# Kernel optimization log

Measured on AMD Instinct MI355X. Metric: run time of the kernel, lower is better.

## Reference

```python
import jax, jax.numpy as jnp
import numpy as np

V, N, K, D = 2, 100000, 8, 128
TAU = 1.0
LOG_2PI = float(np.log(2.0 * np.pi))


def setup_inputs() -> dict:
    key = jax.random.key(0)
    k1, k2, k3 = jax.random.split(key, 3)
    z = jax.random.normal(k1, (V, N, D), dtype=jnp.float32)
    phi = jnp.ones((V, K), dtype=jnp.float32) / K
    mu = jax.random.normal(k2, (V, K, D), dtype=jnp.float32)
    # sigma: identity (as in torch init) plus a small symmetric PSD perturbation
    a = 0.05 * jax.random.normal(k3, (V, K, D, D), dtype=jnp.float32)
    sigma = jnp.eye(D, dtype=jnp.float32) + jnp.einsum('vkde,vkfe->vkdf', a, a)
    return {"z": z, "phi": phi, "mu": mu, "sigma": sigma}


def _compute_energy(z, phi, mu, sigma):
    # z: [N, D]; phi: [K]; mu: [K, D]; sigma: [K, D, D]
    eps_eye = 1e-6 * jnp.eye(D, dtype=z.dtype)
    sigma_stable = sigma + eps_eye  # [K, D, D]
    inv_sigma = jnp.linalg.inv(sigma_stable)
    det_sigma = jnp.clip(jnp.linalg.det(sigma_stable), 1e-6, None)  # [K]
    diff = z[:, None, :] - mu[None, :, :]  # [N, K, D]
    maha = jnp.einsum('nkd,kde,nke->nk', diff, inv_sigma, diff)  # [N, K]
    log_pi = jax.nn.log_softmax(phi)  # [K]
    log_prob = (-0.5 * maha
                - 0.5 * D * LOG_2PI
                - 0.5 * jnp.log(det_sigma)[None, :]
                + log_pi[None, :])  # [N, K]
    energy = -jax.nn.logsumexp(log_prob, axis=1)  # [N]
    penalty = jnp.sum(1.0 / (jnp.diagonal(sigma_stable, axis1=-2, axis2=-1) + 1e-12))
    return energy, penalty


def reference(z, phi, mu, sigma):
    # vmap over views; energies_v: [V, N]
    energies_v, penalties = jax.vmap(_compute_energy)(z, phi, mu, sigma)
    energies = energies_v.T  # [N, V]
    total_energies = jnp.sum(energies)
    total_penalty = jnp.sum(penalties)
    weights = jax.nn.softmax(-energies / TAU, axis=1)  # [N, V]
    return energies, weights, total_energies, total_penalty
```

## Files before the change

### kernel.cpp

```cpp
#include <hip/hip_runtime.h>
#include <math.h>

#define V 2
#define NN 100000
#define KK 8
#define DD 128
#define TILE_N 128
#define SL 132
#define NT 782
#define CH 8
#define NCHUNK 98
#define NPAD 100096
#define LOG2PI 1.8378770664093454f
#define LOG_1EM6 -13.815510557964274f

#define IMG_B 69632
#define IMG_HALF 17408
#define LF_B   1114112
#define BV_B   2228224
#define C_B    2236416
#define MAHA_B 2236480

#define OUT_W_OFF (NN*V)
#define OUT_TE (2*NN*V)
#define OUT_TP (2*NN*V + 1)

typedef __attribute__((ext_vector_type(8))) short bf16x8;
typedef __attribute__((ext_vector_type(4))) float f32x4;

__device__ __forceinline__ unsigned short f2bf_rtn(float f) {
    unsigned u = __builtin_bit_cast(unsigned, f);
    unsigned r = u + 0x7FFFu + ((u >> 16) & 1u);
    return (unsigned short)(r >> 16);
}
__device__ __forceinline__ float bf2f(unsigned short h) {
    unsigned u = ((unsigned)h) << 16;
    return __builtin_bit_cast(float, u);
}

__global__ void zero_kernel(float* out) {
    int t = threadIdx.x;
    if (t < 2) out[OUT_TE + t] = 0.0f;
}

__global__ __launch_bounds__(256) void prep_chol(const float* __restrict__ phi,
                                                 const float* __restrict__ mu,
                                                 const float* __restrict__ sigma,
                                                 void* __restrict__ wsv,
                                                 float* __restrict__ out) {
    __shared__ float Lf[DD * SL];
    __shared__ float P[8][SL];
    __shared__ float dvec[DD];
    __shared__ float mulds[DD];
    __shared__ float red[256];
    __shared__ float Bv[8];
    __shared__ float Bb[DD];

    const int tid = threadIdx.x;
    const int vk  = blockIdx.x;
    const int v   = vk >> 3;
    const int k   = vk & 7;
    const int R   = tid >> 4;
    const int C   = tid & 15;

    if (tid < DD) mulds[tid] = mu[vk * DD + tid];

    float A[8][8];
    const float* sig = sigma + (size_t)vk * DD * DD;
    float pen = 0.0f;
    #pragma unroll
    for (int a = 0; a < 8; ++a) {
        const float4* p4 = (const float4*)(sig + (size_t)(8 * R + a) * DD + 8 * C);
        float4 x = p4[0], y = p4[1];
        A[a][0] = x.x; A[a][1] = x.y; A[a][2] = x.z; A[a][3] = x.w;
        A[a][4] = y.x; A[a][5] = y.y; A[a][6] = y.z; A[a][7] = y.w;
        if (R == C) A[a][a] += 1e-6f;
    }
    if (R == C) {
        #pragma unroll
        for (int a = 0; a < 8; ++a) pen += 1.0f / (A[a][a] + 1e-12f);
    }

    for (int i = tid; i < DD * SL; i += 256) Lf[i] = 0.0f;

    red[tid] = pen;
    __syncthreads();
    for (int s = 128; s > 0; s >>= 1) {
        if (tid < s) red[tid] += red[tid + s];
        __syncthreads();
    }
    if (tid == 0) atomicAdd(&out[OUT_TP], red[0]);
    __syncthreads();

    for (int p = 0; p < 16; ++p) {
        if (C == p && R >= p) {
            #pragma unroll
            for (int b = 0; b < 8; ++b) {
                *(float4*)&P[b][8 * R]     = make_float4(A[0][b], A[1][b], A[2][b], A[3][b]);
                *(float4*)&P[b][8 * R + 4] = make_float4(A[4][b], A[5][b], A[6][b], A[7][b]);
            }
        }
        __syncthreads();

        if (tid < 64) {
            const int lane = tid;
            const int r1 = 8 * p + lane;
            const int r2 = r1 + 64;
            const bool ok2 = (r2 < DD);
            float pr1[8], pr2[8], rs[8];
            #pragma unroll
            for (int j = 0; j < 8; ++j) {
                pr1[j] = (r1 < DD) ? P[j][r1] : 0.0f;
                pr2[j] = ok2 ? P[j][r2] : 0.0f;
            }
            #pragma unroll
            for (int j = 0; j < 8; ++j) {
                if (lane >= j && lane < 8) Bv[lane] = pr1[j];
                __builtin_amdgcn_wave_barrier();
                float bv[8];
                #pragma unroll
                for (int m = 0; m < 8; ++m) bv[m] = Bv[m];
                __builtin_amdgcn_wave_barrier();
                float piv = bv[j];
                if (lane == j) dvec[8 * p + j] = piv;
                float inv2 = 1.0f / piv;
                rs[j] = rsqrtf(piv);
                float m1 = pr1[j] * inv2;
                float m2 = pr2[j] * inv2;
                #pragma unroll
                for (int j2 = 0; j2 < 8; ++j2) {
                    if (j2 > j) {
                        if (lane > j) pr1[j2] -= m1 * bv[j2];
                        pr2[j2] -= m2 * bv[j2];
                    }
                }
            }
            #pragma unroll
            for (int j = 0; j < 8; ++j) {
                if (r1 < DD) {
                    float v1 = (lane >= j) ? pr1[j] * rs[j] : 0.0f;
                    P[j][r1] = v1;
                    Lf[r1 * SL + 8 * p + j] = v1;
                }
                if (ok2) {
                    float v2 = pr2[j] * rs[j];
                    P[j][r2] = v2;
                    Lf[r2 * SL + 8 * p + j] = v2;
                }
            }
        }
        __syncthreads();

        if (C > p && R >= p) {
            #pragma unroll
            for (int j = 0; j < 8; ++j) {
                float4 a0 = *(const float4*)&P[j][8 * R];
                float4 a1 = *(const float4*)&P[j][8 * R + 4];
                float4 b0 = *(const float4*)&P[j][8 * C];
                float4 b1 = *(const float4*)&P[j][8 * C + 4];
                float ra[8] = {a0.x, a0.y, a0.z, a0.w, a1.x, a1.y, a1.z, a1.w};
                float rb[8] = {b0.x, b0.y, b0.z, b0.w, b1.x, b1.y, b1.z, b1.w};
                #pragma unroll
                for (int a = 0; a < 8; ++a)
                    #pragma unroll
                    for (int b = 0; b < 8; ++b)
                        A[a][b] -= ra[a] * rb[b];
            }
        }
        __syncthreads();
    }

    if (tid < 64) {
        const int lane = tid;
        float acc0 = mulds[lane];
        float acc1 = mulds[lane + 64];
        for (int j = 0; j < DD; ++j) {
            if (j < 64) { if (lane == j)      Bb[j] = acc0 / Lf[j * SL + j]; }
            else        { if (lane == j - 64) Bb[j] = acc1 / Lf[j * SL + j]; }
            __builtin_amdgcn_wave_barrier();
            float bj = Bb[j];
            __builtin_amdgcn_wave_barrier();
            if (lane > j)      acc0 -= Lf[lane * SL + j] * bj;
            if (lane + 64 > j) acc1 -= Lf[(lane + 64) * SL + j] * bj;
        }
    }
    __syncthreads();
    if (tid < DD) ((float*)((char*)wsv + BV_B))[vk * DD + tid] = Bb[tid];

    {
        float4* Lg = (float4*)((char*)wsv + LF_B + (size_t)vk * IMG_B);
        const float4* Ls4 = (const float4*)Lf;
        for (int i = tid; i < DD * SL / 4; i += 256) Lg[i] = Ls4[i];
    }

    red[tid] = (tid < DD) ? logf(dvec[tid]) : 0.0f;
    __syncthreads();
    for (int s = 128; s > 0; s >>= 1) {
        if (tid < s) red[tid] += red[tid + s];
        __syncthreads();
    }
    if (tid == 0) {
        float logdet_c = fmaxf(red[0], LOG_1EM6);
        const float* ph = phi + v * KK;
        float m = ph[0];
        for (int i = 1; i < KK; ++i) m = fmaxf(m, ph[i]);
        float s = 0.0f;
        for (int i = 0; i < KK; ++i) s += expf(ph[i] - m);
        float logpi = ph[k] - m - logf(s);
        ((float*)((char*)wsv + C_B))[vk] = logpi - 0.5f * logdet_c - 0.5f * (float)DD * LOG2PI;
    }
}

__global__ __launch_bounds__(256) void prep_trsm(void* __restrict__ wsv) {
    __shared__ float Ls[DD * SL];
    __shared__ float Wc[32][SL];

    const int tid = threadIdx.x;
    const int vk  = blockIdx.x >> 2;
    const int cg  = blockIdx.x & 3;

    const float4* Lg = (const float4*)((const char*)wsv + LF_B + (size_t)vk * IMG_B);
    float4* Ls4 = (float4*)Ls;
    for (int i = tid; i < DD * SL / 4; i += 256) Ls4[i] = Lg[i];
    __syncthreads();

    const int c   = tid >> 3;
    const int par = tid & 7;
    const int j   = 4 * c + cg;

    for (int e = par; e < SL; e += 8) Wc[c][e] = 0.0f;
    if (par == 0) Wc[c][j] = 1.0f / Ls[j * SL + j];
    __builtin_amdgcn_wave_barrier();

    const int pbase = j & ~3;
    for (int i = j + 1; i < DD; ++i) {
        float s = 0.0f;
        for (int p4 = pbase + 4 * par; p4 < i; p4 += 32) {
            float4 lf = *(const float4*)&Ls[i * SL + p4];
            float4 wc = *(const float4*)&Wc[c][p4];
            s += lf.x * wc.x + lf.y * wc.y + lf.z * wc.z + lf.w * wc.w;
        }
        s += __shfl_xor(s, 1, 64);
        s += __shfl_xor(s, 2, 64);
        s += __shfl_xor(s, 4, 64);
        if (par == 0) Wc[c][i] = -s / Ls[i * SL + i];
        __builtin_amdgcn_wave_barrier();
    }

    unsigned short* Gh = (unsigned short*)((char*)wsv + (size_t)vk * IMG_B);
    unsigned short* Gl = Gh + IMG_HALF;
    for (int i2 = par; i2 < DD; i2 += 8) {
        float f = (i2 >= j) ? Wc[c][i2] : 0.0f;
        unsigned short h = f2bf_rtn(f);
        unsigned short l = f2bf_rtn(f - bf2f(h));
        Gh[i2 * 136 + j] = h;
        Gl[i2 * 136 + j] = l;
    }
}

__global__ __launch_bounds__(256, 2) void maha_kernel(const float* __restrict__ z,
                                                      void* __restrict__ wsv) {
    __shared__ unsigned short wl[IMG_B / 2];
    __shared__ float bl_s[DD];

    const int tid  = threadIdx.x;
    const int lane = tid & 63;
    const int wave = tid >> 6;
    const int quad = lane >> 4;
    const int l16  = lane & 15;
    const int r     = blockIdx.y;
    const int chunk = blockIdx.x;
    const int vv    = r >> 3;

    {
        const char* src = (const char*)wsv + (size_t)r * IMG_B;
        char* dst = (char*)wl;
        const int lane_off = wave * 1024 + lane * 16;
        #pragma unroll
        for (int t = 0; t < 17; ++t)
            __builtin_amdgcn_global_load_lds(
                (const __attribute__((address_space(1))) void*)(src + t * 4096 + lane_off),
                (__attribute__((address_space(3))) void*)(dst + t * 4096 + wave * 1024),
                16, 0, 0);
    }
    if (tid < DD) bl_s[tid] = ((const float*)((const char*)wsv + BV_B))[r * DD + tid];
    __syncthreads();

    const float* zbase = z + (size_t)vv * NN * DD;
    float* mrow = (float*)((char*)wsv + MAHA_B) + (size_t)r * NPAD;

    for (int ti = 0; ti < CH; ++ti) {
        const int t = chunk * CH + ti;
        if (t >= NT) break;
        const int n0 = t * TILE_N;

        bf16x8 zhi[2][4], zlo[2][4];
        #pragma unroll
        for (int mt = 0; mt < 2; ++mt) {
            int n = n0 + wave * 32 + mt * 16 + l16;
            bool ok = (n < NN);
            const float* zp = zbase + (size_t)n * DD + quad * 8;
            #pragma unroll
            for (int ds = 0; ds < 4; ++ds) {
                float f[8];
                if (ok) {
                    float4 a  = *(const float4*)(zp + ds * 32);
                    float4 bq = *(const float4*)(zp + ds * 32 + 4);
                    f[0] = a.x;  f[1] = a.y;  f[2] = a.z;  f[3] = a.w;
                    f[4] = bq.x; f[5] = bq.y; f[6] = bq.z; f[7] = bq.w;
                } else {
                    #pragma unroll
                    for (int e = 0; e < 8; ++e) f[e] = 0.0f;
                }
                bf16x8 hi8, lo8;
                #pragma unroll
                for (int e = 0; e < 8; ++e) {
                    unsigned short hu = f2bf_rtn(f[e]);
                    unsigned short lu = f2bf_rtn(f[e] - bf2f(hu));
                    hi8[e] = (short)hu;
                    lo8[e] = (short)lu;
                }
                zhi[mt][ds] = hi8;
                zlo[mt][ds] = lo8;
            }
        }

        f32x4 acc[2][8];
        #pragma unroll
        for (int mt = 0; mt < 2; ++mt)
            #pragma unroll
            for (int nt = 0; nt < 8; ++nt)
                acc[mt][nt] = (f32x4)(0.0f);

        #pragma unroll
        for (int ds = 0; ds < 4; ++ds) {
            const int g = ds * 4 + quad;
            #pragma unroll
            for (int nt = 0; nt < 8; ++nt) {
                if (nt < 2 * ds) continue;
                int row = nt * 16 + l16;
                int off = row * 136 + g * 8;
                bf16x8 bh  = *(const bf16x8*)&wl[off];
                bf16x8 blo = *(const bf16x8*)&wl[IMG_HALF + off];
                #pragma unroll
                for (int mt = 0; mt < 2; ++mt) {
                    acc[mt][nt] = __builtin_amdgcn_mfma_f32_16x16x32_bf16(zhi[mt][ds], bh,  acc[mt][nt], 0, 0, 0);
                    acc[mt][nt] = __builtin_amdgcn_mfma_f32_16x16x32_bf16(zhi[mt][ds], blo, acc[mt][nt], 0, 0, 0);
                    acc[mt][nt] = __builtin_amdgcn_mfma_f32_16x16x32_bf16(zlo[mt][ds], bh,  acc[mt][nt], 0, 0, 0);
                }
            }
        }

        #pragma unroll
        for (int mt = 0; mt < 2; ++mt) {
            float p[4] = {0.f, 0.f, 0.f, 0.f};
            #pragma unroll
            for (int nt = 0; nt < 8; ++nt) {
                float bc = bl_s[nt * 16 + l16];
                f32x4 a = acc[mt][nt];
                float y0 = a[0] - bc, y1 = a[1] - bc, y2 = a[2] - bc, y3 = a[3] - bc;
                p[0] += y0 * y0; p[1] += y1 * y1; p[2] += y2 * y2; p[3] += y3 * y3;
            }
            float sv[4];
            #pragma unroll
            for (int reg = 0; reg < 4; ++reg) {
                float s = p[reg];
                s += __shfl_xor(s, 1, 64);
                s += __shfl_xor(s, 2, 64);
                s += __shfl_xor(s, 4, 64);
                s += __shfl_xor(s, 8, 64);
                sv[reg] = s;
            }
            if (l16 == 0)
                *(float4*)&mrow[n0 + wave * 32 + mt * 16 + quad * 4] =
                    make_float4(sv[0], sv[1], sv[2], sv[3]);
        }
    }
}

__global__ __launch_bounds__(256) void finalize_kernel(const void* __restrict__ wsv,
                                                       float* __restrict__ out) {
    __shared__ float red[256];
    __shared__ float clds[16];

    const int tid = threadIdx.x;
    if (tid < 16) clds[tid] = ((const float*)((const char*)wsv + C_B))[tid];
    __syncthreads();

    const float* mahap = (const float*)((const char*)wsv + MAHA_B);
    const int n = blockIdx.x * 256 + tid;
    float esum = 0.0f;

    if (n < NN) {
        float ev[V];
        #pragma unroll
        for (int vv = 0; vv < V; ++vv) {
            float lp[KK];
            float m = -1e30f;
            #pragma unroll
            for (int k = 0; k < KK; ++k) {
                int r = vv * KK + k;
                lp[k] = -0.5f * mahap[(size_t)r * NPAD + n] + clds[r];
                m = fmaxf(m, lp[k]);
            }
            float s = 0.0f;
            #pragma unroll
            for (int k = 0; k < KK; ++k) s += expf(lp[k] - m);
            ev[vv] = -(m + logf(s));
        }
        float e0 = ev[0], e1 = ev[1];
        float m = fmaxf(-e0, -e1);
        float x0 = expf(-e0 - m);
        float x1 = expf(-e1 - m);
        float inv = 1.0f / (x0 + x1);
        out[(size_t)n * V + 0] = e0;
        out[(size_t)n * V + 1] = e1;
        out[OUT_W_OFF + (size_t)n * V + 0] = x0 * inv;
        out[OUT_W_OFF + (size_t)n * V + 1] = x1 * inv;
        esum = e0 + e1;
    }

    red[tid] = esum;
    __syncthreads();
    for (int s = 128; s > 0; s >>= 1) {
        if (tid < s) red[tid] += red[tid + s];
        __syncthreads();
    }
    if (tid == 0) atomicAdd(&out[OUT_TE], red[0]);
}

extern "C" void kernel_launch(void* const* d_in, const int* in_sizes, int n_in,
                              void* d_out, int out_size, void* d_ws, size_t ws_size,
                              hipStream_t stream) {
    const float* z     = (const float*)d_in[0];
    const float* phi   = (const float*)d_in[1];
    const float* mu    = (const float*)d_in[2];
    const float* sigma = (const float*)d_in[3];
    float* out = (float*)d_out;

    hipLaunchKernelGGL(zero_kernel, dim3(1), dim3(64), 0, stream, out);
    hipLaunchKernelGGL(prep_chol, dim3(V * KK), dim3(256), 0, stream, phi, mu, sigma, d_ws, out);
    hipLaunchKernelGGL(prep_trsm, dim3(64), dim3(256), 0, stream, d_ws);
    hipLaunchKernelGGL(maha_kernel, dim3(NCHUNK, 16), dim3(256), 0, stream, z, d_ws);
    hipLaunchKernelGGL(finalize_kernel, dim3((NPAD + 255) / 256), dim3(256), 0, stream, d_ws, out);
}
```

Measured before the change: 400.3 us.

## Double maha tile to 512 threads, interleave z conversion per k-slice, cheaper bf16 split

The maha kernel now launches 512-thread blocks over 256-row tiles, so each staged LDS image of the triangular factor is reused by twice as many rows, and launch bounds allow four blocks per CU. The z load and bf16 hi/lo split move inside the k-slice loop, which cuts live registers. The split now uses a truncate-plus-round perm sequence instead of two round-to-nearest conversions. This lowers register pressure and conversion ALU work, but the hi part is now truncated, not rounded, which slightly changes numerics. The LDS image copy loop is also rewritten for 8 waves.

```diff
diff --git a/kernel.cpp b/kernel.cpp
--- a/kernel.cpp
+++ b/kernel.cpp
@@ -5,12 +5,12 @@
 #define NN 100000
 #define KK 8
 #define DD 128
-#define TILE_N 128
+#define TILE_N 256
 #define SL 132
-#define NT 782
-#define CH 8
+#define NT 391
+#define CH 4
 #define NCHUNK 98
-#define NPAD 100096
+#define NPAD 100352
 #define LOG2PI 1.8378770664093454f
 #define LOG_1EM6 -13.815510557964274f
 
@@ -27,6 +27,7 @@
 
 typedef __attribute__((ext_vector_type(8))) short bf16x8;
 typedef __attribute__((ext_vector_type(4))) float f32x4;
+typedef __attribute__((ext_vector_type(4))) unsigned u32x4;
 
 __device__ __forceinline__ unsigned short f2bf_rtn(float f) {
     unsigned u = __builtin_bit_cast(unsigned, f);
@@ -36,6 +37,17 @@
 __device__ __forceinline__ float bf2f(unsigned short h) {
     unsigned u = ((unsigned)h) << 16;
     return __builtin_bit_cast(float, u);
+}
+
+__device__ __forceinline__ void cvt_pair(float f0, float f1, unsigned& hi, unsigned& lo) {
+    unsigned u0 = __builtin_bit_cast(unsigned, f0);
+    unsigned u1 = __builtin_bit_cast(unsigned, f1);
+    hi = __builtin_amdgcn_perm(u1, u0, 0x07060302u);
+    float r0 = f0 - __builtin_bit_cast(float, u0 & 0xFFFF0000u);
+    float r1 = f1 - __builtin_bit_cast(float, u1 & 0xFFFF0000u);
+    unsigned v0 = __builtin_bit_cast(unsigned, r0) + 0x8000u;
+    unsigned v1 = __builtin_bit_cast(unsigned, r1) + 0x8000u;
+    lo = __builtin_amdgcn_perm(v1, v0, 0x07060302u);
 }
 
 __global__ void zero_kernel(float* out) {
@@ -258,7 +270,7 @@
     }
 }
 
-__global__ __launch_bounds__(256, 2) void maha_kernel(const float* __restrict__ z,
+__global__ __launch_bounds__(512, 4) void maha_kernel(const float* __restrict__ z,
                                                       void* __restrict__ wsv) {
     __shared__ unsigned short wl[IMG_B / 2];
     __shared__ float bl_s[DD];
@@ -275,13 +287,17 @@
     {
         const char* src = (const char*)wsv + (size_t)r * IMG_B;
         char* dst = (char*)wl;
-        const int lane_off = wave * 1024 + lane * 16;
-        #pragma unroll
-        for (int t = 0; t < 17; ++t)
-            __builtin_amdgcn_global_load_lds(
-                (const __attribute__((address_space(1))) void*)(src + t * 4096 + lane_off),
-                (__attribute__((address_space(3))) void*)(dst + t * 4096 + wave * 1024),
-                16, 0, 0);
+        const int woff = wave * 1024;
+        const int lane_off = woff + lane * 16;
+        #pragma unroll
+        for (int t = 0; t < 9; ++t) {
+            if (t * 8192 + woff < IMG_B) {
+                __builtin_amdgcn_global_load_lds(
+                    (const __attribute__((address_space(1))) void*)(src + t * 8192 + lane_off),
+                    (__attribute__((address_space(3))) void*)(dst + t * 8192 + woff),
+                    16, 0, 0);
+            }
+        }
     }
     if (tid < DD) bl_s[tid] = ((const float*)((const char*)wsv + BV_B))[r * DD + tid];
     __syncthreads();
@@ -290,63 +306,56 @@
     float* mrow = (float*)((char*)wsv + MAHA_B) + (size_t)r * NPAD;
 
     for (int ti = 0; ti < CH; ++ti) {
-        const int t = chunk * CH + ti;
-        if (t >= NT) break;
+        const int t  = chunk * CH + ti;
         const int n0 = t * TILE_N;
 
-        bf16x8 zhi[2][4], zlo[2][4];
-        #pragma unroll
-        for (int mt = 0; mt < 2; ++mt) {
-            int n = n0 + wave * 32 + mt * 16 + l16;
-            bool ok = (n < NN);
-            const float* zp = zbase + (size_t)n * DD + quad * 8;
-            #pragma unroll
-            for (int ds = 0; ds < 4; ++ds) {
+        f32x4 acc[2][8];
+        #pragma unroll
+        for (int mt = 0; mt < 2; ++mt)
+            #pragma unroll
+            for (int nt = 0; nt < 8; ++nt)
+                acc[mt][nt] = (f32x4)(0.0f);
+
+        #pragma unroll
+        for (int ds = 0; ds < 4; ++ds) {
+            u32x4 zh[2], zl[2];
+            #pragma unroll
+            for (int mt = 0; mt < 2; ++mt) {
+                const int n = n0 + wave * 32 + mt * 16 + l16;
                 float f[8];
-                if (ok) {
-                    float4 a  = *(const float4*)(zp + ds * 32);
-                    float4 bq = *(const float4*)(zp + ds * 32 + 4);
+                if (n < NN) {
+                    const float* zp = zbase + (size_t)n * DD + quad * 8 + ds * 32;
+                    float4 a  = *(const float4*)(zp);
+                    float4 bq = *(const float4*)(zp + 4);
                     f[0] = a.x;  f[1] = a.y;  f[2] = a.z;  f[3] = a.w;
                     f[4] = bq.x; f[5] = bq.y; f[6] = bq.z; f[7] = bq.w;
                 } else {
                     #pragma unroll
                     for (int e = 0; e < 8; ++e) f[e] = 0.0f;
                 }
-                bf16x8 hi8, lo8;
                 #pragma unroll
-                for (int e = 0; e < 8; ++e) {
-                    unsigned short hu = f2bf_rtn(f[e]);
-                    unsigned short lu = f2bf_rtn(f[e] - bf2f(hu));
-                    hi8[e] = (short)hu;
-                    lo8[e] = (short)lu;
-                }
-                zhi[mt][ds] = hi8;
-                zlo[mt][ds] = lo8;
-            }
-        }
-
-        f32x4 acc[2][8];
-        #pragma unroll
-        for (int mt = 0; mt < 2; ++mt)
-            #pragma unroll
-            for (int nt = 0; nt < 8; ++nt)
-                acc[mt][nt] = (f32x4)(0.0f);
-
-        #pragma unroll
-        for (int ds = 0; ds < 4; ++ds) {
+                for (int d = 0; d < 4; ++d) {
+                    unsigned hi, lo;
+                    cvt_pair(f[2 * d], f[2 * d + 1], hi, lo);
+                    zh[mt][d] = hi;
+                    zl[mt][d] = lo;
+                }
+            }
+
             const int g = ds * 4 + quad;
             #pragma unroll
-            for (int nt = 0; nt < 8; ++nt) {
-                if (nt < 2 * ds) continue;
-                int row = nt * 16 + l16;
-                int off = row * 136 + g * 8;
+            for (int nt = 2 * ds; nt < 8; ++nt) {
+                const int row = nt * 16 + l16;
+                const int off = row * 136 + g * 8;
                 bf16x8 bh  = *(const bf16x8*)&wl[off];
                 bf16x8 blo = *(const bf16x8*)&wl[IMG_HALF + off];
                 #pragma unroll
                 for (int mt = 0; mt < 2; ++mt) {
-                    acc[mt][nt] = __builtin_amdgcn_mfma_f32_16x16x32_bf16(zhi[mt][ds], bh,  acc[mt][nt], 0, 0, 0);
-                    acc[mt][nt] = __builtin_amdgcn_mfma_f32_16x16x32_bf16(zhi[mt][ds], blo, acc[mt][nt], 0, 0, 0);
-                    acc[mt][nt] = __builtin_amdgcn_mfma_f32_16x16x32_bf16(zlo[mt][ds], bh,  acc[mt][nt], 0, 0, 0);
+                    bf16x8 ah = __builtin_bit_cast(bf16x8, zh[mt]);
+                    bf16x8 al = __builtin_bit_cast(bf16x8, zl[mt]);
+                    acc[mt][nt] = __builtin_amdgcn_mfma_f32_16x16x32_bf16(ah, bh,  acc[mt][nt], 0, 0, 0);
+                    acc[mt][nt] = __builtin_amdgcn_mfma_f32_16x16x32_bf16(ah, blo, acc[mt][nt], 0, 0, 0);
+                    acc[mt][nt] = __builtin_amdgcn_mfma_f32_16x16x32_bf16(al, bh,  acc[mt][nt], 0, 0, 0);
                 }
             }
         }
@@ -441,6 +450,6 @@
     hipLaunchKernelGGL(zero_kernel, dim3(1), dim3(64), 0, stream, out);
     hipLaunchKernelGGL(prep_chol, dim3(V * KK), dim3(256), 0, stream, phi, mu, sigma, d_ws, out);
     hipLaunchKernelGGL(prep_trsm, dim3(64), dim3(256), 0, stream, d_ws);
-    hipLaunchKernelGGL(maha_kernel, dim3(NCHUNK, 16), dim3(256), 0, stream, z, d_ws);
+    hipLaunchKernelGGL(maha_kernel, dim3(NCHUNK, 16), dim3(512), 0, stream, z, d_ws);
     hipLaunchKernelGGL(finalize_kernel, dim3((NPAD + 255) / 256), dim3(256), 0, stream, d_ws, out);
 }
```

Measured after the change: 941.9 us. +135.3%, slower.
